# Performance work log

Measured on AMD Instinct MI355X. Metric: run time of the kernel, lower is better.

The kernel has to match this reference:

```python
import jax, jax.numpy as jnp
import numpy as np

DIM = 640
M_SPATIAL = 100  # 10*10
BATCH = 64
EPS = 1e-5


def setup_inputs() -> dict:
    key = jax.random.key(0)
    kx, = jax.random.split(key, 1)
    x = jax.random.normal(kx, (BATCH, DIM, M_SPATIAL), dtype=jnp.float32)
    # temperature buffer: log(1 / (2 * H * W)) as in BDC.__init__
    t = jnp.log(1.0 / (2.0 * M_SPATIAL) * jnp.ones((1, 1), dtype=jnp.float32))
    return {"x": x, "t": t}


def reference(x, t):
    B, dim, M = x.shape
    # x_pow2 = x @ x^T  -> [B, dim, dim]
    x_pow2 = jnp.einsum('bim,bjm->bij', x, x)
    # I_M.bmm(x_pow2*I) broadcasts diag along rows; (x_pow2*I).bmm(I_M) along cols
    d = jnp.diagonal(x_pow2, axis1=1, axis2=2)  # [B, dim], squared norms
    dcov = d[:, :, None] + d[:, None, :] - 2.0 * x_pow2
    dcov = jnp.clip(dcov, 0.0)
    dcov = jnp.exp(t) * dcov
    dcov = jnp.sqrt(dcov + EPS)
    # double centering: dcov.bmm(I_M) = row sums broadcast, I_M.bmm(dcov) = col sums
    row_mean = jnp.sum(dcov, axis=2, keepdims=True) / dim          # [B, dim, 1]
    col_mean = jnp.sum(dcov, axis=1, keepdims=True) / dim          # [B, 1, dim]
    grand_mean = jnp.sum(dcov, axis=(1, 2), keepdims=True) / (dim * dim)
    bdc = dcov - row_mean - col_mean + grand_mean                   # [B, dim, dim]
    # Triuvec: upper triangle incl. diagonal, row-major order
    iu_r, iu_c = np.triu_indices(dim)
    return bdc[:, iu_r, iu_c]  # [B, dim*(dim+1)//2]
```

## Files before the change

### kernel.cpp

```cpp
#include <hip/hip_runtime.h>
#include <math.h>

#define BATCH 64
#define DIM   640
#define MSP   100
#define TILE  64
#define NT    10
#define NPAIR 55
#define PTRI  205120
#define EPSV  1e-5f

#define WS_D 0
#define WS_S 40960
#define WS_G 81920
#define XB_OFF 327936ull
#define TI_OFF 10813696ull


typedef __attribute__((ext_vector_type(8))) short short8;
typedef __attribute__((ext_vector_type(4))) float f32x4;
typedef __attribute__((ext_vector_type(2))) __fp16 fp16x2;

__device__ __forceinline__ short f2bf(float f) {
    union { float f; unsigned u; } x; x.f = f;
    unsigned r = x.u + 0x7fffu + ((x.u >> 16) & 1u);
    return (short)(r >> 16);
}
__device__ __forceinline__ float bf2f(short h) {
    union { unsigned u; float f; } x; x.u = ((unsigned)(unsigned short)h) << 16;
    return x.f;
}

__device__ __forceinline__ void decode_pair(int u, int& ti, int& tj) {
    ti = 0;
    while (u >= NT - ti) { u -= NT - ti; ++ti; }
    tj = ti + u;
}

__global__ __launch_bounds__(256) void k_prep(const float* __restrict__ x,
                                              float* __restrict__ ws) {
    short* xb = (short*)((char*)ws + XB_OFF);
    const int t = threadIdx.x;
    const int rr = t >> 4, c = t & 15;
    const int row = blockIdx.x * 16 + rr;
    const int k0 = c * 8;
    const float* src = x + (size_t)row * MSP;

    float v[8];
#pragma unroll
    for (int e = 0; e < 8; ++e) v[e] = 0.f;
    if (k0 <= 88) {
        float4 u0 = *(const float4*)(src + k0);
        float4 u1 = *(const float4*)(src + k0 + 4);
        v[0] = u0.x; v[1] = u0.y; v[2] = u0.z; v[3] = u0.w;
        v[4] = u1.x; v[5] = u1.y; v[6] = u1.z; v[7] = u1.w;
    } else if (k0 == 96) {
        float4 u0 = *(const float4*)(src + 96);
        v[0] = u0.x; v[1] = u0.y; v[2] = u0.z; v[3] = u0.w;
    }

    short8 h; float s = 0.f;
#pragma unroll
    for (int e = 0; e < 8; ++e) {
        short hb = f2bf(v[e]);
        float vr = bf2f(hb);
        s += vr * vr;
        h[e] = hb;
    }
    *(short8*)(xb + (size_t)blockIdx.x * 2048 + c * 128 + rr * 8) = h;

    s += __shfl_xor(s, 1); s += __shfl_xor(s, 2);
    s += __shfl_xor(s, 4); s += __shfl_xor(s, 8);
    if (c == 0) { ws[WS_D + row] = s; ws[WS_S + row] = 0.f; }
    if (blockIdx.x == 0 && t < BATCH) ws[WS_G + t] = 0.f;
}

__global__ __launch_bounds__(256) void k_gram(const float* __restrict__ tsc,
                                              float* __restrict__ ws) {
    __shared__ float sRow[TILE];
    __shared__ float sCol[TILE];

    int ti, tj;
    decode_pair(blockIdx.x, ti, tj);
    const int b = blockIdx.y;
    const int i0 = ti * TILE, j0 = tj * TILE;
    const int tid = threadIdx.x;
    const short* xb = (const short*)((const char*)ws + XB_OFF);

    if (tid < TILE) { sRow[tid] = 0.f; sCol[tid] = 0.f; }

    const int wave = tid >> 6, lane = tid & 63;
    const int lm = lane & 15, lq = lane >> 4;
    const int r0 = (wave >> 1) * 32, c0 = (wave & 1) * 32;

    const short* pa = xb + (size_t)(b * 40 + ((i0 + r0) >> 4)) * 2048 + lq * 128 + lm * 8;
    const short* pb = xb + (size_t)(b * 40 + ((j0 + c0) >> 4)) * 2048 + lq * 128 + lm * 8;

    f32x4 acc[2][2] = {};
#pragma unroll
    for (int ks = 0; ks < 4; ++ks) {
        short8 a0 = *(const short8*)(pa + ks * 512);
        short8 a1 = *(const short8*)(pa + 2048 + ks * 512);
        short8 b0 = *(const short8*)(pb + ks * 512);
        short8 b1 = *(const short8*)(pb + 2048 + ks * 512);
        acc[0][0] = __builtin_amdgcn_mfma_f32_16x16x32_bf16(a0, b0, acc[0][0], 0, 0, 0);
        acc[0][1] = __builtin_amdgcn_mfma_f32_16x16x32_bf16(a0, b1, acc[0][1], 0, 0, 0);
        acc[1][0] = __builtin_amdgcn_mfma_f32_16x16x32_bf16(a1, b0, acc[1][0], 0, 0, 0);
        acc[1][1] = __builtin_amdgcn_mfma_f32_16x16x32_bf16(a1, b1, acc[1][1], 0, 0, 0);
    }

    const float scale = expf(tsc[0]);
    const float* dn = ws + WS_D + b * DIM;
    float di[2][4], dj[2];
#pragma unroll
    for (int a = 0; a < 2; ++a)
#pragma unroll
        for (int r = 0; r < 4; ++r) di[a][r] = dn[i0 + r0 + 16 * a + lq * 4 + r];
#pragma unroll
    for (int bb = 0; bb < 2; ++bb) dj[bb] = dn[j0 + c0 + 16 * bb + lm];

    float rp[2][4] = {}, cp[2] = {};
    short* tb = (short*)((char*)ws + TI_OFF) + ((size_t)(b * NPAIR + blockIdx.x) << 12);
    uint4 st[2];
#pragma unroll
    for (int a = 0; a < 2; ++a) {
        unsigned wd[4];
#pragma unroll
        for (int bb = 0; bb < 2; ++bb)
#pragma unroll
            for (int p = 0; p < 2; ++p) {
                float d0 = di[a][2 * p]     + dj[bb];
                float d1 = di[a][2 * p + 1] + dj[bb];
                float v0 = __builtin_amdgcn_sqrtf(
                    fmaf(scale, fmaxf(fmaf(-2.f, acc[a][bb][2 * p],     d0), 0.f), EPSV));
                float v1 = __builtin_amdgcn_sqrtf(
                    fmaf(scale, fmaxf(fmaf(-2.f, acc[a][bb][2 * p + 1], d1), 0.f), EPSV));
                rp[a][2 * p] += v0; rp[a][2 * p + 1] += v1; cp[bb] += v0 + v1;
                union { fp16x2 h; unsigned u; } cv;
                cv.h = __builtin_amdgcn_cvt_pkrtz(v0, v1);
                wd[bb * 2 + p] = cv.u;
            }
        st[a].x = wd[0]; st[a].y = wd[1]; st[a].z = wd[2]; st[a].w = wd[3];
    }
    *(uint4*)(tb + tid * 16)     = st[0];
    *(uint4*)(tb + tid * 16 + 8) = st[1];

    __syncthreads();
#pragma unroll
    for (int a = 0; a < 2; ++a)
#pragma unroll
        for (int r = 0; r < 4; ++r) {
            float v = rp[a][r];
            v += __shfl_xor(v, 1); v += __shfl_xor(v, 2);
            v += __shfl_xor(v, 4); v += __shfl_xor(v, 8);
            if (lm == 0) atomicAdd(&sRow[r0 + 16 * a + lq * 4 + r], v);
        }
#pragma unroll
    for (int bb = 0; bb < 2; ++bb) {
        float v = cp[bb];
        v += __shfl_xor(v, 16); v += __shfl_xor(v, 32);
        if (lq == 0) atomicAdd(&sCol[c0 + 16 * bb + lm], v);
    }
    __syncthreads();

    float* S = ws + WS_S + b * DIM;
    if (tid < TILE) {
        atomicAdd(&S[i0 + tid], sRow[tid]);
        if (ti != tj) atomicAdd(&S[j0 + tid], sCol[tid]);
        float gg = sRow[tid];
        gg += __shfl_xor(gg, 1);  gg += __shfl_xor(gg, 2);  gg += __shfl_xor(gg, 4);
        gg += __shfl_xor(gg, 8);  gg += __shfl_xor(gg, 16); gg += __shfl_xor(gg, 32);
        if (tid == 0) atomicAdd(&ws[WS_G + b], (ti == tj ? 1.f : 2.f) * gg);
    }
}

__global__ __launch_bounds__(256) void k_final(const float* __restrict__ ws,
                                               float* __restrict__ out) {
    int ti, tj;
    decode_pair(blockIdx.x, ti, tj);
    const int b = blockIdx.y;
    const int i0 = ti * TILE, j0 = tj * TILE;
    const int tid = threadIdx.x;
    const int wave = tid >> 6, lane = tid & 63;
    const int lm = lane & 15, lq = lane >> 4;
    const int r0 = (wave >> 1) * 32, c0 = (wave & 1) * 32;

    const uint4* tb = (const uint4*)((const char*)ws + TI_OFF +
                                     ((size_t)(b * NPAIR + blockIdx.x) << 13));
    uint4 u[2];
    u[0] = tb[tid * 2]; u[1] = tb[tid * 2 + 1];

    const float inv = 1.f / (float)DIM;
    const float g = ws[WS_G + b] * (inv * inv);
    const float* S = ws + WS_S + b * DIM;

    float ai[2][4]; int ib[2][4];
#pragma unroll
    for (int a = 0; a < 2; ++a)
#pragma unroll
        for (int r = 0; r < 4; ++r) {
            int i = i0 + r0 + 16 * a + 4 * lq + r;
            ai[a][r] = g - S[i] * inv;
            ib[a][r] = i * DIM - (i * (i - 1)) / 2 - i;
        }
    float bj[2]; int jj[2];
#pragma unroll
    for (int bb = 0; bb < 2; ++bb) {
        int j = j0 + c0 + 16 * bb + lm;
        jj[bb] = j; bj[bb] = -S[j] * inv;
    }

    const bool offd = (ti != tj);
    float* outb = out + (size_t)b * PTRI;
#pragma unroll
    for (int a = 0; a < 2; ++a) {
        unsigned wd[4] = {u[a].x, u[a].y, u[a].z, u[a].w};
        const int ibase = i0 + r0 + 16 * a + 4 * lq;
#pragma unroll
        for (int bb = 0; bb < 2; ++bb)
#pragma unroll
            for (int p = 0; p < 2; ++p) {
                union { unsigned u; fp16x2 h; } cv; cv.u = wd[bb * 2 + p];
                float v0 = (float)cv.h.x, v1 = (float)cv.h.y;
                const int r = 2 * p;
                if (offd || jj[bb] >= ibase + r)
                    outb[ib[a][r] + jj[bb]] = v0 + ai[a][r] + bj[bb];
                if (offd || jj[bb] >= ibase + r + 1)
                    outb[ib[a][r + 1] + jj[bb]] = v1 + ai[a][r + 1] + bj[bb];
            }
    }
}

extern "C" void kernel_launch(void* const* d_in, const int* in_sizes, int n_in,
                              void* d_out, int out_size, void* d_ws, size_t ws_size,
                              hipStream_t stream) {
    const float* x = (const float*)d_in[0];
    const float* t = (const float*)d_in[1];
    float* out = (float*)d_out;
    float* ws  = (float*)d_ws;

    k_prep <<<dim3(BATCH * DIM / 16), 256, 0, stream>>>(x, ws);
    k_gram <<<dim3(NPAIR, BATCH),     256, 0, stream>>>(t, ws);
    k_final<<<dim3(NPAIR, BATCH),     256, 0, stream>>>(ws, out);
}
```

Before: 129.9 us.

## Recompute Gram tiles in write pass instead of storing fp16 intermediate

The sums kernel no longer writes the fp16 distance tiles to workspace, and the write kernel recomputes the bf16 MFMA Gram tile and the sqrt distance from the prepared x instead of reading them back. This removes roughly 29 MB of intermediate global write plus read traffic in exchange for running the small K=128 matmul twice. Output values now come from fp32 distances rather than fp16-rounded ones, which also slightly changes numerics.

```diff
diff --git a/kernel.cpp b/kernel.cpp
--- a/kernel.cpp
+++ b/kernel.cpp
@@ -14,12 +14,10 @@
 #define WS_S 40960
 #define WS_G 81920
 #define XB_OFF 327936ull
-#define TI_OFF 10813696ull
 
 
 typedef __attribute__((ext_vector_type(8))) short short8;
 typedef __attribute__((ext_vector_type(4))) float f32x4;
-typedef __attribute__((ext_vector_type(2))) __fp16 fp16x2;
 
 __device__ __forceinline__ short f2bf(float f) {
     union { float f; unsigned u; } x; x.f = f;
@@ -75,7 +73,7 @@
     if (blockIdx.x == 0 && t < BATCH) ws[WS_G + t] = 0.f;
 }
 
-__global__ __launch_bounds__(256) void k_gram(const float* __restrict__ tsc,
+__global__ __launch_bounds__(256) void k_sums(const float* __restrict__ tsc,
                                               float* __restrict__ ws) {
     __shared__ float sRow[TILE];
     __shared__ float sCol[TILE];
@@ -120,11 +118,8 @@
     for (int bb = 0; bb < 2; ++bb) dj[bb] = dn[j0 + c0 + 16 * bb + lm];
 
     float rp[2][4] = {}, cp[2] = {};
-    short* tb = (short*)((char*)ws + TI_OFF) + ((size_t)(b * NPAIR + blockIdx.x) << 12);
-    uint4 st[2];
-#pragma unroll
-    for (int a = 0; a < 2; ++a) {
-        unsigned wd[4];
+#pragma unroll
+    for (int a = 0; a < 2; ++a)
 #pragma unroll
         for (int bb = 0; bb < 2; ++bb)
 #pragma unroll
@@ -136,14 +131,7 @@
                 float v1 = __builtin_amdgcn_sqrtf(
                     fmaf(scale, fmaxf(fmaf(-2.f, acc[a][bb][2 * p + 1], d1), 0.f), EPSV));
                 rp[a][2 * p] += v0; rp[a][2 * p + 1] += v1; cp[bb] += v0 + v1;
-                union { fp16x2 h; unsigned u; } cv;
-                cv.h = __builtin_amdgcn_cvt_pkrtz(v0, v1);
-                wd[bb * 2 + p] = cv.u;
             }
-        st[a].x = wd[0]; st[a].y = wd[1]; st[a].z = wd[2]; st[a].w = wd[3];
-    }
-    *(uint4*)(tb + tid * 16)     = st[0];
-    *(uint4*)(tb + tid * 16 + 8) = st[1];
 
     __syncthreads();
 #pragma unroll
@@ -174,57 +162,77 @@
     }
 }
 
-__global__ __launch_bounds__(256) void k_final(const float* __restrict__ ws,
+__global__ __launch_bounds__(256) void k_write(const float* __restrict__ tsc,
+                                               const float* __restrict__ ws,
                                                float* __restrict__ out) {
     int ti, tj;
     decode_pair(blockIdx.x, ti, tj);
     const int b = blockIdx.y;
     const int i0 = ti * TILE, j0 = tj * TILE;
     const int tid = threadIdx.x;
+    const short* xb = (const short*)((const char*)ws + XB_OFF);
+
     const int wave = tid >> 6, lane = tid & 63;
     const int lm = lane & 15, lq = lane >> 4;
     const int r0 = (wave >> 1) * 32, c0 = (wave & 1) * 32;
 
-    const uint4* tb = (const uint4*)((const char*)ws + TI_OFF +
-                                     ((size_t)(b * NPAIR + blockIdx.x) << 13));
-    uint4 u[2];
-    u[0] = tb[tid * 2]; u[1] = tb[tid * 2 + 1];
-
+    const short* pa = xb + (size_t)(b * 40 + ((i0 + r0) >> 4)) * 2048 + lq * 128 + lm * 8;
+    const short* pb = xb + (size_t)(b * 40 + ((j0 + c0) >> 4)) * 2048 + lq * 128 + lm * 8;
+
+    f32x4 acc[2][2] = {};
+#pragma unroll
+    for (int ks = 0; ks < 4; ++ks) {
+        short8 a0 = *(const short8*)(pa + ks * 512);
+        short8 a1 = *(const short8*)(pa + 2048 + ks * 512);
+        short8 b0 = *(const short8*)(pb + ks * 512);
+        short8 b1 = *(const short8*)(pb + 2048 + ks * 512);
+        acc[0][0] = __builtin_amdgcn_mfma_f32_16x16x32_bf16(a0, b0, acc[0][0], 0, 0, 0);
+        acc[0][1] = __builtin_amdgcn_mfma_f32_16x16x32_bf16(a0, b1, acc[0][1], 0, 0, 0);
+        acc[1][0] = __builtin_amdgcn_mfma_f32_16x16x32_bf16(a1, b0, acc[1][0], 0, 0, 0);
+        acc[1][1] = __builtin_amdgcn_mfma_f32_16x16x32_bf16(a1, b1, acc[1][1], 0, 0, 0);
+    }
+
+    const float scale = expf(tsc[0]);
     const float inv = 1.f / (float)DIM;
     const float g = ws[WS_G + b] * (inv * inv);
-    const float* S = ws + WS_S + b * DIM;
-
-    float ai[2][4]; int ib[2][4];
+    const float* S  = ws + WS_S + b * DIM;
+    const float* dn = ws + WS_D + b * DIM;
+
+    float di[2][4], ai[2][4]; int ib[2][4];
 #pragma unroll
     for (int a = 0; a < 2; ++a)
 #pragma unroll
         for (int r = 0; r < 4; ++r) {
             int i = i0 + r0 + 16 * a + 4 * lq + r;
+            di[a][r] = dn[i];
             ai[a][r] = g - S[i] * inv;
             ib[a][r] = i * DIM - (i * (i - 1)) / 2 - i;
         }
-    float bj[2]; int jj[2];
+    float dj[2], bj[2]; int jj[2];
 #pragma unroll
     for (int bb = 0; bb < 2; ++bb) {
         int j = j0 + c0 + 16 * bb + lm;
-        jj[bb] = j; bj[bb] = -S[j] * inv;
+        jj[bb] = j; dj[bb] = dn[j]; bj[bb] = -S[j] * inv;
     }
 
     const bool offd = (ti != tj);
     float* outb = out + (size_t)b * PTRI;
 #pragma unroll
     for (int a = 0; a < 2; ++a) {
-        unsigned wd[4] = {u[a].x, u[a].y, u[a].z, u[a].w};
         const int ibase = i0 + r0 + 16 * a + 4 * lq;
 #pragma unroll
         for (int bb = 0; bb < 2; ++bb)
 #pragma unroll
             for (int p = 0; p < 2; ++p) {
-                union { unsigned u; fp16x2 h; } cv; cv.u = wd[bb * 2 + p];
-                float v0 = (float)cv.h.x, v1 = (float)cv.h.y;
                 const int r = 2 * p;
+                float d0 = di[a][r]     + dj[bb];
+                float d1 = di[a][r + 1] + dj[bb];
+                float v0 = __builtin_amdgcn_sqrtf(
+                    fmaf(scale, fmaxf(fmaf(-2.f, acc[a][bb][r],     d0), 0.f), EPSV));
+                float v1 = __builtin_amdgcn_sqrtf(
+                    fmaf(scale, fmaxf(fmaf(-2.f, acc[a][bb][r + 1], d1), 0.f), EPSV));
                 if (offd || jj[bb] >= ibase + r)
-                    outb[ib[a][r] + jj[bb]] = v0 + ai[a][r] + bj[bb];
+                    outb[ib[a][r]     + jj[bb]] = v0 + ai[a][r]     + bj[bb];
                 if (offd || jj[bb] >= ibase + r + 1)
                     outb[ib[a][r + 1] + jj[bb]] = v1 + ai[a][r + 1] + bj[bb];
             }
@@ -240,6 +248,6 @@
     float* ws  = (float*)d_ws;
 
     k_prep <<<dim3(BATCH * DIM / 16), 256, 0, stream>>>(x, ws);
-    k_gram <<<dim3(NPAIR, BATCH),     256, 0, stream>>>(t, ws);
-    k_final<<<dim3(NPAIR, BATCH),     256, 0, stream>>>(ws, out);
-}
+    k_sums <<<dim3(NPAIR, BATCH),     256, 0, stream>>>(t, ws);
+    k_write<<<dim3(NPAIR, BATCH),     256, 0, stream>>>(t, ws, out);
+}
```

Measured after the change: 140.5 us. 8.2% more time.
